# Optimization experiments

Measured on AMD Instinct MI355X. Metric: run time of the kernel, lower is better.

## Reference

```python
import jax, jax.numpy as jnp
import numpy as np

B, S, VOCAB, D_MODEL, N_KERNELS, KSIZE, N_CLASSES = 8, 2048, 32000, 512, 256, 9, 4096
PAD = KSIZE // 2  # source uses kernel_size/2 (py2 int div)


def setup_inputs() -> dict:
    key = jax.random.key(0)
    ks = jax.random.split(key, 7)
    return {
        "text": jax.random.randint(ks[0], (B, S), 0, VOCAB),
        "embed_table": jax.random.normal(ks[1], (VOCAB, D_MODEL), dtype=jnp.float32) * 0.02,
        "conv_w": jax.random.normal(ks[2], (N_KERNELS, D_MODEL, KSIZE), dtype=jnp.float32) * 0.02,
        "conv_b": jax.random.normal(ks[3], (N_KERNELS,), dtype=jnp.float32) * 0.02,
        "U_w": jax.random.normal(ks[4], (N_CLASSES, N_KERNELS), dtype=jnp.float32) * 0.02,
        "final_w": jax.random.normal(ks[5], (N_CLASSES, N_KERNELS), dtype=jnp.float32) * 0.02,
        "final_b": jax.random.normal(ks[6], (N_CLASSES,), dtype=jnp.float32) * 0.02,
    }


def reference(text, embed_table, conv_w, conv_b, U_w, final_w, final_b):
    # Embedding lookup (tgt_embed); dropout is identity in eval mode.
    x = embed_table[text]                                  # [B, S, D]
    # Conv1d over sequence: NCH layout, OIH kernel, same-length padding.
    xc = jax.lax.conv_general_dilated(
        x.transpose(0, 2, 1), conv_w,
        window_strides=(1,), padding=[(PAD, PAD)],
        dimension_numbers=("NCH", "OIH", "NCH"))
    x = jnp.tanh(xc.transpose(0, 2, 1) + conv_b)           # [B, S, K]
    # Shared-query label attention: scores [B, n_classes, S].
    scores = jnp.einsum("ck,bsk->bcs", U_w, x)
    alpha = jax.nn.softmax(scores, axis=2)
    m = jnp.einsum("bcs,bsk->bck", alpha, x)               # [B, C, K]
    y = jnp.sum(final_w * m, axis=2) + final_b             # [B, C]
    return y
```

## Files before the change

kernel.cpp:

```cpp
#include <hip/hip_runtime.h>
#include <math.h>

#define B 8
#define S 2048
#define D_MODEL 512
#define NK 256
#define KSZ 9
#define NC 4096
#define PADW 4
#define SSPLIT 4
#define CM 64
#define CW (CM + 8)
#define LRS 520
#define DCH 32
#define NSTG (KSZ * (D_MODEL / DCH))
#define NTILES ((S / SSPLIT) / 32)

typedef __attribute__((ext_vector_type(8))) short bf16x8;
typedef __attribute__((ext_vector_type(4))) float f32x4;

static __device__ __forceinline__ unsigned short f2bf(float f) {
    unsigned int u = __float_as_uint(f);
    unsigned int r = (u + 0x7fffu + ((u >> 16) & 1u)) >> 16;
    return (unsigned short)r;
}

#define GLOAD_LDS16(g, l) __builtin_amdgcn_global_load_lds( \
    (const __attribute__((address_space(1))) void*)(g),     \
    (__attribute__((address_space(3))) void*)(l), 16, 0, 0)

#define PREP_W (KSZ * NK * D_MODEL)
#define PREP_UF (NC * NK)
__global__ __launch_bounds__(256) void prep_all(
    const float* __restrict__ w, unsigned short* __restrict__ wtb,
    const float* __restrict__ U, unsigned short* __restrict__ Ub,
    const float* __restrict__ F, unsigned short* __restrict__ Fb)
{
    int idx = blockIdx.x * 256 + threadIdx.x;
    if (idx < PREP_W) {
        int d = idx % D_MODEL;
        int k = (idx / D_MODEL) % NK;
        int t = idx / (D_MODEL * NK);
        wtb[idx] = f2bf(w[((size_t)k * D_MODEL + d) * KSZ + t]);
        return;
    }
    idx -= PREP_W;
    if (idx < PREP_UF) { Ub[idx] = f2bf(U[idx]); return; }
    idx -= PREP_UF;
    if (idx < PREP_UF) { Fb[idx] = f2bf(F[idx]); }
}

__global__ __launch_bounds__(512, 2) void conv_mfma(
    const int* __restrict__ text, const float* __restrict__ emb,
    const unsigned short* __restrict__ wtb, const float* __restrict__ bias,
    unsigned short* __restrict__ xf)
{
    __shared__ unsigned short xs[CW * LRS];
    __shared__ unsigned short wls[2 * NK * DCH];
    const int b  = blockIdx.x >> 5;
    const int s0 = (blockIdx.x & 31) * CM;
    const int tid = threadIdx.x;

    for (int i = tid; i < CW * (D_MODEL / 4); i += 512) {
        int row = i >> 7;
        int c4  = i & 127;
        int gs = s0 + row - PADW;
        float4 v = make_float4(0.f, 0.f, 0.f, 0.f);
        if (gs >= 0 && gs < S) {
            int tok = text[b * S + gs];
            v = ((const float4*)(emb + (size_t)tok * D_MODEL))[c4];
        }
        ushort4 o;
        o.x = f2bf(v.x); o.y = f2bf(v.y); o.z = f2bf(v.z); o.w = f2bf(v.w);
        *(ushort4*)(xs + row * LRS + c4 * 4) = o;
    }

    #define WSTAGE(bb, stg)                                                   \
        {                                                                     \
            int t_ = (stg) >> 4, h_ = (stg) & 15;                             \
            _Pragma("unroll")                                                 \
            for (int j = 0; j < 2; j++) {                                     \
                int C = j * 512 + tid;                                        \
                int k_ = C >> 2;                                              \
                int jl = (C & 3) ^ ((C >> 3) & 3);                            \
                const unsigned short* src =                                   \
                    wtb + ((size_t)(t_ * NK + k_)) * D_MODEL + h_ * DCH + jl * 8; \
                unsigned short* dst = wls + (bb) * (NK * DCH) + C * 8;        \
                GLOAD_LDS16(src, dst);                                        \
            }                                                                 \
        }

    WSTAGE(0, 0)

    const int wv   = tid >> 6;
    const int lane = tid & 63;
    const int cl   = lane & 15;
    const int quad = lane >> 4;
    const int n0   = wv * 32;
    const int jp   = quad ^ ((cl >> 1) & 3);

    f32x4 acc[4][2] = {};

    for (int stg = 0; stg < NSTG; stg++) {
        __syncthreads();
        if (stg + 1 < NSTG) WSTAGE((stg + 1) & 1, stg + 1)

        const int t = stg >> 4, h = stg & 15;
        const unsigned short* wb = wls + (stg & 1) * (NK * DCH);
        const unsigned short* ap = xs + (cl + t) * LRS + h * DCH + quad * 8;

        bf16x8 b0 = *(const bf16x8*)(wb + (n0 + cl) * DCH + jp * 8);
        bf16x8 b1 = *(const bf16x8*)(wb + (n0 + 16 + cl) * DCH + jp * 8);
        #pragma unroll
        for (int ms = 0; ms < 4; ms++) {
            bf16x8 a = *(const bf16x8*)(ap + ms * 16 * LRS);
            acc[ms][0] = __builtin_amdgcn_mfma_f32_16x16x32_bf16(a, b0, acc[ms][0], 0, 0, 0);
            acc[ms][1] = __builtin_amdgcn_mfma_f32_16x16x32_bf16(a, b1, acc[ms][1], 0, 0, 0);
        }
    }

    #pragma unroll
    for (int ns = 0; ns < 2; ns++) {
        const int k = n0 + ns * 16 + cl;
        const float bk = bias[k];
        #pragma unroll
        for (int ms = 0; ms < 4; ms++) {
            #pragma unroll
            for (int r = 0; r < 4; r++) {
                int s = s0 + ms * 16 + quad * 4 + r;
                float v = acc[ms][ns][r] + bk;
                float e = __expf(2.f * v);
                float th = 1.f - 2.f / (e + 1.f);
                xf[((size_t)b * S + s) * NK + k] = f2bf(th);
            }
        }
    }
}

__global__ __launch_bounds__(256, 2) void attn_mfma(
    const unsigned short* __restrict__ xf, const unsigned short* __restrict__ Ub,
    const unsigned short* __restrict__ Fb, float* __restrict__ pm,
    float* __restrict__ pl, float* __restrict__ pg)
{
    __shared__ unsigned short xsa[2 * 32 * NK];
    const int b    = blockIdx.z;
    const int sp   = blockIdx.y;
    const int tid  = threadIdx.x;
    const int wv   = tid >> 6;
    const int lane = tid & 63;
    const int cl   = lane & 15;
    const int quad = lane >> 4;
    const int c0   = blockIdx.x * 128 + wv * 32;
    const int wvu  = __builtin_amdgcn_readfirstlane(wv);

    bf16x8 uf[2][8], ff[2][8];
    #pragma unroll
    for (int cg = 0; cg < 2; cg++) {
        const unsigned short* up = Ub + (size_t)(c0 + cg * 16 + cl) * NK + quad * 8;
        const unsigned short* fp = Fb + (size_t)(c0 + cg * 16 + cl) * NK + quad * 8;
        #pragma unroll
        for (int kk = 0; kk < 8; kk++) {
            uf[cg][kk] = *(const bf16x8*)(up + kk * 32);
            ff[cg][kk] = *(const bf16x8*)(fp + kk * 32);
        }
    }

    const int sbeg = sp * (S / SSPLIT);
    const unsigned short* xb = xf + ((size_t)b * S + sbeg) * NK;

    #define STAGE(bb, t)                                                      \
        {                                                                     \
            _Pragma("unroll")                                                 \
            for (int j = 0; j < 4; j++) {                                     \
                int C = j * 256 + tid;                                        \
                int r = C >> 5, p = C & 31;                                   \
                int jl = p ^ (r & 7);                                         \
                const unsigned short* src = xb + (size_t)((t) * 32 + r) * NK + jl * 8; \
                unsigned short* dst = xsa + (bb) * 8192 + j * 2048 + wvu * 512; \
                GLOAD_LDS16(src, dst);                                        \
            }                                                                 \
        }

    STAGE(0, 0)

    float m[2] = {-1e30f, -1e30f}, l[2] = {0.f, 0.f}, G[2] = {0.f, 0.f};
    const int swz = cl & 7;

    for (int t = 0; t < NTILES; t++) {
        __syncthreads();
        if (t + 1 < NTILES) STAGE((t + 1) & 1, t + 1)

        const unsigned short* bs = xsa + (t & 1) * 8192;
        f32x4 sa[2][2] = {}, ga[2][2] = {};
        #pragma unroll
        for (int kk = 0; kk < 8; kk++) {
            int p0 = (quad + 4 * kk) ^ swz;
            bf16x8 a0 = *(const bf16x8*)(bs + cl * NK + p0 * 8);
            bf16x8 a1 = *(const bf16x8*)(bs + (16 + cl) * NK + p0 * 8);
            #pragma unroll
            for (int cg = 0; cg < 2; cg++) {
                sa[0][cg] = __builtin_amdgcn_mfma_f32_16x16x32_bf16(a0, uf[cg][kk], sa[0][cg], 0, 0, 0);
                ga[0][cg] = __builtin_amdgcn_mfma_f32_16x16x32_bf16(a0, ff[cg][kk], ga[0][cg], 0, 0, 0);
                sa[1][cg] = __builtin_amdgcn_mfma_f32_16x16x32_bf16(a1, uf[cg][kk], sa[1][cg], 0, 0, 0);
                ga[1][cg] = __builtin_amdgcn_mfma_f32_16x16x32_bf16(a1, ff[cg][kk], ga[1][cg], 0, 0, 0);
            }
        }

        #pragma unroll
        for (int cg = 0; cg < 2; cg++) {
            float tm = fmaxf(fmaxf(fmaxf(sa[0][cg][0], sa[0][cg][1]), fmaxf(sa[0][cg][2], sa[0][cg][3])),
                             fmaxf(fmaxf(sa[1][cg][0], sa[1][cg][1]), fmaxf(sa[1][cg][2], sa[1][cg][3])));
            tm = fmaxf(tm, __shfl_xor(tm, 16));
            tm = fmaxf(tm, __shfl_xor(tm, 32));
            float mn = fmaxf(m[cg], tm);
            float sc = __expf(m[cg] - mn);
            l[cg] *= sc; G[cg] *= sc; m[cg] = mn;
            #pragma unroll
            for (int r = 0; r < 4; r++) {
                float e0 = __expf(sa[0][cg][r] - mn);
                float e1 = __expf(sa[1][cg][r] - mn);
                l[cg] += e0 + e1;
                G[cg] += e0 * ga[0][cg][r] + e1 * ga[1][cg][r];
            }
        }
    }

    #pragma unroll
    for (int cg = 0; cg < 2; cg++) {
        l[cg] += __shfl_xor(l[cg], 16); l[cg] += __shfl_xor(l[cg], 32);
        G[cg] += __shfl_xor(G[cg], 16); G[cg] += __shfl_xor(G[cg], 32);
    }
    if (lane < 16) {
        #pragma unroll
        for (int cg = 0; cg < 2; cg++) {
            size_t idx = ((size_t)b * SSPLIT + sp) * NC + c0 + cg * 16 + lane;
            pm[idx] = m[cg]; pl[idx] = l[cg]; pg[idx] = G[cg];
        }
    }
}

__global__ __launch_bounds__(256) void combine_kernel(
    const float* __restrict__ pm, const float* __restrict__ pl,
    const float* __restrict__ pg, const float* __restrict__ fb,
    float* __restrict__ out)
{
    int idx = blockIdx.x * 256 + threadIdx.x;
    if (idx >= B * NC) return;
    int b = idx / NC, c = idx % NC;
    float mm = -1e30f;
    #pragma unroll
    for (int sp = 0; sp < SSPLIT; sp++)
        mm = fmaxf(mm, pm[((size_t)b * SSPLIT + sp) * NC + c]);
    float l = 0.f, g = 0.f;
    #pragma unroll
    for (int sp = 0; sp < SSPLIT; sp++) {
        size_t i = ((size_t)b * SSPLIT + sp) * NC + c;
        float e = __expf(pm[i] - mm);
        l += pl[i] * e;
        g += pg[i] * e;
    }
    out[idx] = g / l + fb[c];
}

extern "C" void kernel_launch(void* const* d_in, const int* in_sizes, int n_in,
                              void* d_out, int out_size, void* d_ws, size_t ws_size,
                              hipStream_t stream) {
    const int*   text   = (const int*)  d_in[0];
    const float* emb    = (const float*)d_in[1];
    const float* conv_w = (const float*)d_in[2];
    const float* conv_b = (const float*)d_in[3];
    const float* U_w    = (const float*)d_in[4];
    const float* F_w    = (const float*)d_in[5];
    const float* f_b    = (const float*)d_in[6];
    float* out = (float*)d_out;

    char* ws = (char*)d_ws;
    unsigned short* xf  = (unsigned short*)ws; ws += (size_t)B * S * NK * 2;
    unsigned short* wtb = (unsigned short*)ws; ws += (size_t)KSZ * NK * D_MODEL * 2;
    unsigned short* Ub  = (unsigned short*)ws; ws += (size_t)NC * NK * 2;
    unsigned short* Fb  = (unsigned short*)ws; ws += (size_t)NC * NK * 2;
    float* pm = (float*)ws; ws += (size_t)SSPLIT * B * NC * 4;
    float* pl = (float*)ws; ws += (size_t)SSPLIT * B * NC * 4;
    float* pg = (float*)ws; ws += (size_t)SSPLIT * B * NC * 4;

    const int prep_n = PREP_W + 2 * PREP_UF;
    prep_all<<<dim3((prep_n + 255) / 256), 256, 0, stream>>>(conv_w, wtb, U_w, Ub, F_w, Fb);
    conv_mfma<<<dim3(B * S / CM), 512, 0, stream>>>(text, emb, wtb, conv_b, xf);
    attn_mfma<<<dim3(NC / 128, SSPLIT, B), 256, 0, stream>>>(xf, Ub, Fb, pm, pl, pg);
    combine_kernel<<<dim3((B * NC + 255) / 256), 256, 0, stream>>>(pm, pl, pg, f_b, out);
}
```

Baseline: 261.1 us.

## Stream conv weights from global into registers with double-buffering, drop LDS weight staging

The conv kernel no longer stages weights through LDS with per-stage barriers. Each wave now loads its B fragments directly from global memory into registers, with a two-deep software pipeline. The activation tile in LDS switches from row padding to an XOR swizzle. Blocks grow to 1024 threads, with waves split over two M-groups of 32 rows. This removes the 144 barriers per block and the LDS weight traffic, but weights are now re-read from global/L2 by every wave, and register pressure rises under the 1024-thread launch bounds.

Result: slower. 302.1 us (+15.7%).

```diff
diff --git a/kernel.cpp b/kernel.cpp
--- a/kernel.cpp
+++ b/kernel.cpp
@@ -11,9 +11,7 @@
 #define SSPLIT 4
 #define CM 64
 #define CW (CM + 8)
-#define LRS 520
-#define DCH 32
-#define NSTG (KSZ * (D_MODEL / DCH))
+#define NSTG (KSZ * 16)
 #define NTILES ((S / SSPLIT) / 32)
 
 typedef __attribute__((ext_vector_type(8))) short bf16x8;
@@ -50,73 +48,77 @@
     if (idx < PREP_UF) { Fb[idx] = f2bf(F[idx]); }
 }
 
-__global__ __launch_bounds__(512, 2) void conv_mfma(
+__global__ __launch_bounds__(1024, 4) void conv_mfma(
     const int* __restrict__ text, const float* __restrict__ emb,
     const unsigned short* __restrict__ wtb, const float* __restrict__ bias,
     unsigned short* __restrict__ xf)
 {
-    __shared__ unsigned short xs[CW * LRS];
-    __shared__ unsigned short wls[2 * NK * DCH];
+    __shared__ unsigned short xs[CW * D_MODEL];
     const int b  = blockIdx.x >> 5;
     const int s0 = (blockIdx.x & 31) * CM;
     const int tid = threadIdx.x;
 
-    for (int i = tid; i < CW * (D_MODEL / 4); i += 512) {
-        int row = i >> 7;
-        int c4  = i & 127;
-        int gs = s0 + row - PADW;
-        float4 v = make_float4(0.f, 0.f, 0.f, 0.f);
-        if (gs >= 0 && gs < S) {
-            int tok = text[b * S + gs];
-            v = ((const float4*)(emb + (size_t)tok * D_MODEL))[c4];
-        }
-        ushort4 o;
-        o.x = f2bf(v.x); o.y = f2bf(v.y); o.z = f2bf(v.z); o.w = f2bf(v.w);
-        *(ushort4*)(xs + row * LRS + c4 * 4) = o;
-    }
-
-    #define WSTAGE(bb, stg)                                                   \
-        {                                                                     \
-            int t_ = (stg) >> 4, h_ = (stg) & 15;                             \
-            _Pragma("unroll")                                                 \
-            for (int j = 0; j < 2; j++) {                                     \
-                int C = j * 512 + tid;                                        \
-                int k_ = C >> 2;                                              \
-                int jl = (C & 3) ^ ((C >> 3) & 3);                            \
-                const unsigned short* src =                                   \
-                    wtb + ((size_t)(t_ * NK + k_)) * D_MODEL + h_ * DCH + jl * 8; \
-                unsigned short* dst = wls + (bb) * (NK * DCH) + C * 8;        \
-                GLOAD_LDS16(src, dst);                                        \
-            }                                                                 \
-        }
-
-    WSTAGE(0, 0)
+    #pragma unroll
+    for (int it = 0; it < 5; it++) {
+        int u = it * 1024 + tid;
+        if (u < CW * 64) {
+            int row = u >> 6, c = u & 63;
+            int gs = s0 + row - PADW;
+            float4 v0 = make_float4(0.f, 0.f, 0.f, 0.f), v1 = v0;
+            if (gs >= 0 && gs < S) {
+                int tok = text[b * S + gs];
+                const float4* e4 = (const float4*)(emb + (size_t)tok * D_MODEL + c * 8);
+                v0 = e4[0]; v1 = e4[1];
+            }
+            union { bf16x8 v; unsigned short us[8]; } pk;
+            pk.us[0] = f2bf(v0.x); pk.us[1] = f2bf(v0.y);
+            pk.us[2] = f2bf(v0.z); pk.us[3] = f2bf(v0.w);
+            pk.us[4] = f2bf(v1.x); pk.us[5] = f2bf(v1.y);
+            pk.us[6] = f2bf(v1.z); pk.us[7] = f2bf(v1.w);
+            int phys = c ^ (row & 7);
+            *(bf16x8*)(xs + row * D_MODEL + phys * 8) = pk.v;
+        }
+    }
+    __syncthreads();
 
     const int wv   = tid >> 6;
     const int lane = tid & 63;
     const int cl   = lane & 15;
     const int quad = lane >> 4;
-    const int n0   = wv * 32;
-    const int jp   = quad ^ ((cl >> 1) & 3);
-
-    f32x4 acc[4][2] = {};
-
-    for (int stg = 0; stg < NSTG; stg++) {
-        __syncthreads();
-        if (stg + 1 < NSTG) WSTAGE((stg + 1) & 1, stg + 1)
-
-        const int t = stg >> 4, h = stg & 15;
-        const unsigned short* wb = wls + (stg & 1) * (NK * DCH);
-        const unsigned short* ap = xs + (cl + t) * LRS + h * DCH + quad * 8;
-
-        bf16x8 b0 = *(const bf16x8*)(wb + (n0 + cl) * DCH + jp * 8);
-        bf16x8 b1 = *(const bf16x8*)(wb + (n0 + 16 + cl) * DCH + jp * 8);
-        #pragma unroll
-        for (int ms = 0; ms < 4; ms++) {
-            bf16x8 a = *(const bf16x8*)(ap + ms * 16 * LRS);
-            acc[ms][0] = __builtin_amdgcn_mfma_f32_16x16x32_bf16(a, b0, acc[ms][0], 0, 0, 0);
-            acc[ms][1] = __builtin_amdgcn_mfma_f32_16x16x32_bf16(a, b1, acc[ms][1], 0, 0, 0);
-        }
+    const int mg   = wv & 1;
+    const int n0   = (wv >> 1) * 32;
+    const int arow = mg * 32 + cl;
+
+    bf16x8 aC[2], bC[2], aN[2], bN[2];
+    f32x4 acc[2][2] = {};
+
+    #define LDSTG(AA, BB, stg)                                                \
+        {                                                                     \
+            int t_ = (stg) >> 4, h_ = (stg) & 15;                             \
+            const unsigned short* wp =                                        \
+                wtb + ((size_t)(t_ * NK + n0 + cl)) * D_MODEL + h_ * 32 + quad * 8; \
+            BB[0] = *(const bf16x8*)(wp);                                     \
+            BB[1] = *(const bf16x8*)(wp + 16 * D_MODEL);                      \
+            _Pragma("unroll")                                                 \
+            for (int ms = 0; ms < 2; ms++) {                                  \
+                int row = arow + ms * 16 + t_;                                \
+                int ph  = (h_ * 4 + quad) ^ (row & 7);                        \
+                AA[ms] = *(const bf16x8*)(xs + row * D_MODEL + ph * 8);       \
+            }                                                                 \
+        }
+    #define DOMFMA(AA, BB)                                                    \
+        _Pragma("unroll")                                                     \
+        for (int ms = 0; ms < 2; ms++) {                                      \
+            acc[ms][0] = __builtin_amdgcn_mfma_f32_16x16x32_bf16(AA[ms], BB[0], acc[ms][0], 0, 0, 0); \
+            acc[ms][1] = __builtin_amdgcn_mfma_f32_16x16x32_bf16(AA[ms], BB[1], acc[ms][1], 0, 0, 0); \
+        }
+
+    LDSTG(aC, bC, 0)
+    for (int ss = 0; ss < NSTG; ss += 2) {
+        LDSTG(aN, bN, ss + 1)
+        DOMFMA(aC, bC)
+        if (ss + 2 < NSTG) LDSTG(aC, bC, ss + 2)
+        DOMFMA(aN, bN)
     }
 
     #pragma unroll
@@ -124,10 +126,10 @@
         const int k = n0 + ns * 16 + cl;
         const float bk = bias[k];
         #pragma unroll
-        for (int ms = 0; ms < 4; ms++) {
+        for (int ms = 0; ms < 2; ms++) {
             #pragma unroll
             for (int r = 0; r < 4; r++) {
-                int s = s0 + ms * 16 + quad * 4 + r;
+                int s = s0 + mg * 32 + ms * 16 + quad * 4 + r;
                 float v = acc[ms][ns][r] + bk;
                 float e = __expf(2.f * v);
                 float th = 1.f - 2.f / (e + 1.f);
@@ -285,7 +287,7 @@
 
     const int prep_n = PREP_W + 2 * PREP_UF;
     prep_all<<<dim3((prep_n + 255) / 256), 256, 0, stream>>>(conv_w, wtb, U_w, Ub, F_w, Fb);
-    conv_mfma<<<dim3(B * S / CM), 512, 0, stream>>>(text, emb, wtb, conv_b, xf);
+    conv_mfma<<<dim3(B * S / CM), 1024, 0, stream>>>(text, emb, wtb, conv_b, xf);
     attn_mfma<<<dim3(NC / 128, SSPLIT, B), 256, 0, stream>>>(xf, Ub, Fb, pm, pl, pg);
     combine_kernel<<<dim3((B * NC + 255) / 256), 256, 0, stream>>>(pm, pl, pg, f_b, out);
 }
```
